# Optimization experiments

Hardware: AMD Instinct MI355X
Metric: run time of the kernel (lower is better)

## Reference

```python
import jax, jax.numpy as jnp
import numpy as np

B, T, NM = 128, 2048, 8  # batch, nSteps, nMaxwell


def setup_inputs() -> dict:
    key = jax.random.key(0)
    k1, k2, k3 = jax.random.split(key, 3)
    S_e = jax.random.normal(k1, (B, T, 3, 3), dtype=jnp.float32)
    # strictly increasing times per batch element
    dt = jax.random.uniform(k2, (B, T), minval=0.01, maxval=0.1, dtype=jnp.float32)
    t = jnp.cumsum(dt, axis=1)
    # [tau_1..tau_nM, g_infy, g_1..g_nM] -> last dim 2*NM + 1
    PronyParams = jax.random.uniform(k3, (B, T, 2 * NM + 1), minval=0.1, maxval=1.0, dtype=jnp.float32)
    return {"S_e": S_e, "t": t, "PronyParams": PronyParams}


def reference(S_e, t, PronyParams):
    """Viscoelastic 2nd Piola-Kirchhoff stress via recursive Prony update.

    S_e:         [B, T, 3, 3] instantaneous elastic stress
    t:           [B, T] time
    PronyParams: [B, T, 2*nM+1] (relaxation times tau then coefficients g)
    Returns (S, S_infy, Q_sum), each [B, T, 3, 3].
    """
    nM = PronyParams.shape[-1] // 2
    tau = PronyParams[..., :nM]                      # [B,T,nM]
    g = PronyParams[..., nM:]                        # [B,T,nM+1]
    g = g / jnp.sum(g, axis=-1, keepdims=True)
    g_infy = g[..., 0:1]                             # [B,T,1]
    g_i = g[..., 1:]                                 # [B,T,nM]

    Bsz = S_e.shape[0]
    # time-major scan inputs
    xs = (
        jnp.swapaxes(t, 0, 1),      # [T,B]
        jnp.swapaxes(S_e, 0, 1),    # [T,B,3,3]
        jnp.swapaxes(tau, 0, 1),    # [T,B,nM]
        jnp.swapaxes(g_i, 0, 1),    # [T,B,nM]
    )
    init = (
        jnp.zeros((Bsz, nM, 3, 3), S_e.dtype),  # Q_0
        -t[:, 1],                                # t_prev (as in original initializer)
        jnp.zeros((Bsz, 3, 3), S_e.dtype),       # S_prev
        tau[:, 0],
        g_i[:, 0],
    )

    def step(carry, x):
        Q_p, t_p, S_p, tau_p, g_p = carry
        t_c, S_c, tau_c, g_c = x
        g_bar = 0.5 * (g_c + g_p)                 # [B,nM]
        tau_bar = 0.5 * (tau_c + tau_p)           # [B,nM]
        dt = (t_c - t_p)[:, None]                 # [B,1]
        e = jnp.exp(-0.5 * dt / tau_bar)          # exp(-dt/(2 tau_bar))
        term1 = (e * e)[..., None, None]          # exp(-dt/tau_bar), [B,nM,1,1]
        term2 = (e * g_bar)[..., None, None]      # [B,nM,1,1]
        dS = (S_c - S_p)[:, None]                 # [B,1,3,3]
        Q = term1 * Q_p + term2 * dS              # [B,nM,3,3]
        return (Q, t_c, S_c, tau_c, g_c), Q

    _, Qs = jax.lax.scan(step, init, xs)          # [T,B,nM,3,3]
    Q_sum = jnp.swapaxes(jnp.sum(Qs, axis=2), 0, 1)  # [B,T,3,3]
    S_infy = g_infy[..., None] * S_e              # [B,T,1,1] * [B,T,3,3]
    S = S_infy + Q_sum
    return (S, S_infy, Q_sum)
```

## Files before the change

### kernel.cpp

```cpp
#include <hip/hip_runtime.h>

#define T_LEN 2048
#define NMODE 8
#define NPP   17

template <int L, int G>
__global__ __launch_bounds__(256, 8)
void fused(const float* __restrict__ Se,
           const float* __restrict__ tt,
           const float* __restrict__ pp,
           float* __restrict__ out,
           float* __restrict__ spine,
           unsigned* __restrict__ flags,
           unsigned* __restrict__ ticket,
           int B) {
    constexpr int NSTEP = G * L;
    constexpr int TILES = T_LEN / NSTEP;
    constexpr int RW    = NSTEP + 1;
    constexpr int NT    = 256;
    constexpr int RAW_SZ = RW * NPP;
    constexpr int SROW   = NSTEP + 4;
    constexpr int QT_SZ  = 9 * SROW;
    constexpr int CA_K   = L * 8 + 4;
    constexpr int UNION_SZ = (RAW_SZ > QT_SZ + G * CA_K) ? RAW_SZ
                                                         : (QT_SZ + G * CA_K);
    constexpr int AC_K  = L * 16 + 4;
    constexpr int O_AC  = UNION_SZ;
    constexpr int OV_ZREL = 0;
    constexpr int OV_PP   = G * 72;
    constexpr int OV_Z    = OV_PP + G * 8;
    constexpr int OV_R    = OV_Z + G * 72;
    constexpr int OV_P    = OV_R + G * 72;
    static_assert(OV_P + G * 8 <= G * AC_K, "overlay fits in AC region");
    constexpr int O_T   = O_AC + G * AC_K;
    constexpr int O_INV = O_T + RW;
    constexpr int O_GI  = O_INV + RW;
    constexpr int TOTAL = O_GI + RW;
    static_assert(TOTAL * 4 <= 20480, "LDS must allow 8 blocks/CU");
    static_assert(L == 16, "epilogue uses t>>4 / t&15");

    __shared__ __align__(16) float sm[TOTAL];
    float* s_raw  = sm;
    float* s_qT   = sm;
    float* s_ca   = sm + QT_SZ;
    float* s_AC   = sm + O_AC;
    float* s_Zrel = sm + O_AC + OV_ZREL;
    float* s_Pp   = sm + O_AC + OV_PP;
    float* s_Z    = sm + O_AC + OV_Z;
    float* s_R    = sm + O_AC + OV_R;
    float* s_P    = sm + O_AC + OV_P;
    float* s_t    = sm + O_T;
    float* s_inv  = sm + O_INV;
    float* s_gi   = sm + O_GI;

    const int tid = threadIdx.x;

    __shared__ unsigned s_vid;
    if (tid == 0) s_vid = atomicAdd(ticket, 1u);
    __syncthreads();
    const int vid  = (int)(s_vid % (unsigned)(B * TILES));
    const int tile = vid / B;
    const int b    = vid % B;

    const int base = tile * NSTEP;
    const int off  = (base == 0) ? 0 : 1;
    const int r0   = (base == 0) ? 0 : base - 1;

    {
        const float* pr = pp + ((size_t)b * T_LEN + r0) * NPP;
        for (int i = tid; i < RW * NPP; i += NT) s_raw[i] = pr[i];
        const float* tr = tt + (size_t)b * T_LEN + r0;
        for (int i = tid; i < RW; i += NT) s_t[i] = tr[i];
    }
    __syncthreads();

    for (int i = tid; i < RW; i += NT) {
        float gs = 0.f;
        #pragma unroll
        for (int k = 8; k < NPP; ++k) gs += s_raw[i * NPP + k];
        float iv = __builtin_amdgcn_rcpf(gs);
        s_inv[i] = iv;
        s_gi[i]  = s_raw[i * NPP + 8] * iv;
    }
    __syncthreads();

    for (int i = tid; i < NSTEP * 8; i += NT) {
        int m  = i & 7;
        int ts = i >> 3;
        int rc = ts + off;
        bool first = (base == 0) && (ts == 0);
        int rp = first ? rc : rc - 1;
        float tau_c = s_raw[rc * NPP + m];
        float tau_p = s_raw[rp * NPP + m];
        float gqh_c = 0.5f * s_raw[rc * NPP + 9 + m] * s_inv[rc];
        float gqh_p = 0.5f * s_raw[rp * NPP + 9 + m] * s_inv[rp];
        float t_c = s_t[rc];
        float t_p = first ? -s_t[1] : s_t[rp];
        float ee  = __expf((t_p - t_c) * __builtin_amdgcn_rcpf(tau_c + tau_p));
        int kk = ts / L, sl = ts % L;
        s_AC[kk * AC_K + sl * 16 + m]     = ee * ee;
        s_AC[kk * AC_K + sl * 16 + 8 + m] = ee * (gqh_c + gqh_p);
    }
    __syncthreads();

    float Q[8] = {0,0,0,0,0,0,0,0};
    float cumA_c = 1.f;
    if (tid < 72) {
        const int k = tid / 9;
        const int e = tid - k * 9;
        const float* Sg = Se + (size_t)b * T_LEN * 9 + e;
        const int gbase = base + k * L;

        float dS[L];
        {
            float prev = (base == 0 && k == 0) ? 0.f
                                               : Sg[(size_t)(gbase - 1) * 9];
            #pragma unroll
            for (int s = 0; s < L; ++s) {
                float cur = Sg[(size_t)(gbase + s) * 9];
                dS[s] = cur - prev;
                prev = cur;
            }
        }

        const float4* acp = (const float4*)(s_AC + k * AC_K);
        #pragma unroll
        for (int s = 0; s < L; ++s) {
            float4 a0 = acp[4*s], a1 = acp[4*s+1];
            float4 c0v = acp[4*s+2], c1v = acp[4*s+3];
            float d = dS[s];
            Q[0] = a0.x*Q[0] + c0v.x*d;  Q[1] = a0.y*Q[1] + c0v.y*d;
            Q[2] = a0.z*Q[2] + c0v.z*d;  Q[3] = a0.w*Q[3] + c0v.w*d;
            Q[4] = a1.x*Q[4] + c1v.x*d;  Q[5] = a1.y*Q[5] + c1v.y*d;
            Q[6] = a1.z*Q[6] + c1v.z*d;  Q[7] = a1.w*Q[7] + c1v.w*d;
            float qs = ((Q[0]+Q[1])+(Q[2]+Q[3])) + ((Q[4]+Q[5])+(Q[6]+Q[7]));
            s_qT[e * SROW + (k * L + s)] = qs;
        }
    } else if (tid >= 192) {
        const int u = tid - 192;
        const int k = u >> 3;
        const int m = u & 7;
        #pragma unroll
        for (int s = 0; s < L; ++s) {
            cumA_c *= s_AC[k * AC_K + s * 16 + m];
            s_ca[k * CA_K + s * 8 + m] = cumA_c;
        }
    }
    __syncthreads();

    if (tid < 72) {
        float4* r4 = (float4*)(s_R + 8 * tid);
        r4[0] = make_float4(Q[0], Q[1], Q[2], Q[3]);
        r4[1] = make_float4(Q[4], Q[5], Q[6], Q[7]);
    } else if (tid >= 192) {
        s_P[tid - 192] = cumA_c;
    }
    __syncthreads();

    if (tid < 72) {
        const int e = tid >> 3;
        const int m = tid & 7;
        float z = 0.f, pprod = 1.f;
        #pragma unroll
        for (int k = 0; k < G; ++k) {
            s_Zrel[k * 72 + tid] = z;
            if (e == 0) s_Pp[k * 8 + m] = pprod;
            float Pk = s_P[k * 8 + m];
            z = Pk * z + s_R[k * 72 + tid];
            pprod *= Pk;
        }
        if (tile != TILES - 1) {
            float* sp = spine + ((size_t)b * TILES + tile) * 80;
            __hip_atomic_store(sp + 8 + tid, z, __ATOMIC_RELAXED,
                               __HIP_MEMORY_SCOPE_AGENT);
            if (e == 0)
                __hip_atomic_store(sp + m, pprod, __ATOMIC_RELAXED,
                                   __HIP_MEMORY_SCOPE_AGENT);
        }
    }
    if (tile != TILES - 1)
        asm volatile("s_waitcnt vmcnt(0)" ::: "memory");
    __syncthreads();

    if (tile != TILES - 1 && tid == 0)
        __hip_atomic_store(&flags[(size_t)b * TILES + tile], 1u,
                           __ATOMIC_RELAXED, __HIP_MEMORY_SCOPE_AGENT);

    const size_t nOut = (size_t)B * T_LEN * 9;
    float* o0 = out + ((size_t)b * T_LEN + base) * 9;
    float* o1 = o0 + nOut;
    float* o2 = o0 + 2 * nOut;
    const float4* sv4 = (const float4*)(Se + ((size_t)b * T_LEN + base) * 9);
    for (int i4 = tid; i4 < NSTEP * 9 / 4; i4 += NT) {
        float4 sv = sv4[i4];
        int i = i4 * 4;
        float f0 = s_gi[(i    ) / 9 + off] * sv.x;
        float f1 = s_gi[(i + 1) / 9 + off] * sv.y;
        float f2 = s_gi[(i + 2) / 9 + off] * sv.z;
        float f3 = s_gi[(i + 3) / 9 + off] * sv.w;
        ((float4*)o1)[i4] = make_float4(f0, f1, f2, f3);
    }

    if (tile > 0 && tid < 64) {
        bool done = (tid >= tile);
        while (!__all(done)) {
            if (!done) {
                unsigned f = __hip_atomic_load(
                    &flags[(size_t)b * TILES + tid],
                    __ATOMIC_RELAXED, __HIP_MEMORY_SCOPE_AGENT);
                done = (f != 0u);
                if (!done) __builtin_amdgcn_s_sleep(1);
            }
        }
    }
    __syncthreads();

    float zin = 0.f;
    if (tid < 72 && tile > 0) {
        const int m = tid & 7;
        const float* spb = spine + (size_t)b * TILES * 80;
        float Pv[TILES - 1], Rv[TILES - 1];
        #pragma unroll
        for (int j = 0; j < TILES - 1; ++j) {
            if (j < tile) {
                Pv[j] = __hip_atomic_load(spb + j * 80 + m,
                                          __ATOMIC_RELAXED,
                                          __HIP_MEMORY_SCOPE_AGENT);
                Rv[j] = __hip_atomic_load(spb + j * 80 + 8 + tid,
                                          __ATOMIC_RELAXED,
                                          __HIP_MEMORY_SCOPE_AGENT);
            }
        }
        #pragma unroll
        for (int j = 0; j < TILES - 1; ++j)
            if (j < tile) zin = Pv[j] * zin + Rv[j];
    }

    if (tid < 72) {
        const int m = tid & 7;
        #pragma unroll
        for (int k = 0; k < G; ++k)
            s_Z[k * 72 + tid] = s_Pp[k * 8 + m] * zin + s_Zrel[k * 72 + tid];
    }
    __syncthreads();

    for (int i4 = tid; i4 < NSTEP * 9 / 4; i4 += NT) {
        float4 sv = sv4[i4];
        const float svc[4] = {sv.x, sv.y, sv.z, sv.w};
        int i = i4 * 4;
        float q[4], f[4];
        #pragma unroll
        for (int j = 0; j < 4; ++j) {
            int idx = i + j;
            int t = idx / 9, e = idx - t * 9;
            int rc = t + off;
            int k = t >> 4, s = t & 15;
            const float* caT = &s_ca[k * CA_K + s * 8];
            const float* zE  = &s_Z[k * 72 + e * 8];
            float cr = 0.f;
            #pragma unroll
            for (int m = 0; m < NMODE; ++m) cr += caT[m] * zE[m];
            q[j] = s_qT[e * SROW + t] + cr;
            f[j] = s_gi[rc] * svc[j];
        }
        ((float4*)o2)[i4] = make_float4(q[0], q[1], q[2], q[3]);
        ((float4*)o0)[i4] = make_float4(f[0]+q[0], f[1]+q[1],
                                        f[2]+q[2], f[3]+q[3]);
    }
}

extern "C" void kernel_launch(void* const* d_in, const int* in_sizes, int n_in,
                              void* d_out, int out_size, void* d_ws, size_t ws_size,
                              hipStream_t stream) {
    const float* Se = (const float*)d_in[0];
    const float* tt = (const float*)d_in[1];
    const float* pp = (const float*)d_in[2];
    float* out = (float*)d_out;

    int B = in_sizes[1] / T_LEN;

    constexpr int L = 16;
    constexpr int G = 8;
    constexpr int NSTEP = G * L;
    constexpr int TILES = T_LEN / NSTEP;

    unsigned* ticket = (unsigned*)d_ws;
    unsigned* flags  = ticket + 1;
    size_t ctl_bytes = (size_t)(1 + B * TILES) * sizeof(unsigned);
    size_t spine_off = (ctl_bytes + 15) & ~(size_t)15;
    float* spine = (float*)((char*)d_ws + spine_off);

    hipMemsetAsync(d_ws, 0, ctl_bytes, stream);

    fused<L, G><<<B * TILES, dim3(256), 0, stream>>>(
        Se, tt, pp, out, spine, flags, ticket, B);
}
```

Measured before the change: 118.9 us.

## Overlap S_infy output with scan, stripe ticket atomics, drop LDS param staging

```diff
diff --git a/kernel.cpp b/kernel.cpp
--- a/kernel.cpp
+++ b/kernel.cpp
@@ -18,29 +18,24 @@
     constexpr int TILES = T_LEN / NSTEP;
     constexpr int RW    = NSTEP + 1;
     constexpr int NT    = 256;
-    constexpr int RAW_SZ = RW * NPP;
-    constexpr int SROW   = NSTEP + 4;
-    constexpr int QT_SZ  = 9 * SROW;
-    constexpr int CA_K   = L * 8 + 4;
-    constexpr int UNION_SZ = (RAW_SZ > QT_SZ + G * CA_K) ? RAW_SZ
-                                                         : (QT_SZ + G * CA_K);
+    constexpr int SROW  = NSTEP + 4;
+    constexpr int QT_SZ = 9 * SROW;
+    constexpr int CA_K  = L * 8 + 4;
     constexpr int AC_K  = L * 16 + 4;
-    constexpr int O_AC  = UNION_SZ;
+    constexpr int O_AC  = QT_SZ + G * CA_K;
     constexpr int OV_ZREL = 0;
     constexpr int OV_PP   = G * 72;
     constexpr int OV_Z    = OV_PP + G * 8;
     constexpr int OV_R    = OV_Z + G * 72;
     constexpr int OV_P    = OV_R + G * 72;
     static_assert(OV_P + G * 8 <= G * AC_K, "overlay fits in AC region");
-    constexpr int O_T   = O_AC + G * AC_K;
-    constexpr int O_INV = O_T + RW;
+    constexpr int O_INV = O_AC + G * AC_K;
     constexpr int O_GI  = O_INV + RW;
     constexpr int TOTAL = O_GI + RW;
     static_assert(TOTAL * 4 <= 20480, "LDS must allow 8 blocks/CU");
     static_assert(L == 16, "epilogue uses t>>4 / t&15");
 
     __shared__ __align__(16) float sm[TOTAL];
-    float* s_raw  = sm;
     float* s_qT   = sm;
     float* s_ca   = sm + QT_SZ;
     float* s_AC   = sm + O_AC;
@@ -49,14 +44,17 @@
     float* s_Z    = sm + O_AC + OV_Z;
     float* s_R    = sm + O_AC + OV_R;
     float* s_P    = sm + O_AC + OV_P;
-    float* s_t    = sm + O_T;
     float* s_inv  = sm + O_INV;
     float* s_gi   = sm + O_GI;
 
     const int tid = threadIdx.x;
 
     __shared__ unsigned s_vid;
-    if (tid == 0) s_vid = atomicAdd(ticket, 1u);
+    if (tid == 0) {
+        unsigned stripe = (unsigned)blockIdx.x & 7u;
+        unsigned idx = atomicAdd(&ticket[stripe], 1u);
+        s_vid = idx * 8u + stripe;
+    }
     __syncthreads();
     const int vid  = (int)(s_vid % (unsigned)(B * TILES));
     const int tile = vid / B;
@@ -66,21 +64,17 @@
     const int off  = (base == 0) ? 0 : 1;
     const int r0   = (base == 0) ? 0 : base - 1;
 
-    {
-        const float* pr = pp + ((size_t)b * T_LEN + r0) * NPP;
-        for (int i = tid; i < RW * NPP; i += NT) s_raw[i] = pr[i];
-        const float* tr = tt + (size_t)b * T_LEN + r0;
-        for (int i = tid; i < RW; i += NT) s_t[i] = tr[i];
-    }
-    __syncthreads();
+    const float* ppb = pp + ((size_t)b * T_LEN + r0) * NPP;
+    const float* ttb = tt + (size_t)b * T_LEN + r0;
 
     for (int i = tid; i < RW; i += NT) {
+        const float* gp = ppb + i * NPP + 8;
         float gs = 0.f;
         #pragma unroll
-        for (int k = 8; k < NPP; ++k) gs += s_raw[i * NPP + k];
+        for (int k = 0; k < 9; ++k) gs += gp[k];
         float iv = __builtin_amdgcn_rcpf(gs);
         s_inv[i] = iv;
-        s_gi[i]  = s_raw[i * NPP + 8] * iv;
+        s_gi[i]  = gp[0] * iv;
     }
     __syncthreads();
 
@@ -90,18 +84,24 @@
         int rc = ts + off;
         bool first = (base == 0) && (ts == 0);
         int rp = first ? rc : rc - 1;
-        float tau_c = s_raw[rc * NPP + m];
-        float tau_p = s_raw[rp * NPP + m];
-        float gqh_c = 0.5f * s_raw[rc * NPP + 9 + m] * s_inv[rc];
-        float gqh_p = 0.5f * s_raw[rp * NPP + 9 + m] * s_inv[rp];
-        float t_c = s_t[rc];
-        float t_p = first ? -s_t[1] : s_t[rp];
+        float tau_c = ppb[rc * NPP + m];
+        float tau_p = ppb[rp * NPP + m];
+        float gqh_c = 0.5f * ppb[rc * NPP + 9 + m] * s_inv[rc];
+        float gqh_p = 0.5f * ppb[rp * NPP + 9 + m] * s_inv[rp];
+        float t_c = ttb[rc];
+        float t_p = first ? -ttb[1] : ttb[rp];
         float ee  = __expf((t_p - t_c) * __builtin_amdgcn_rcpf(tau_c + tau_p));
         int kk = ts / L, sl = ts % L;
         s_AC[kk * AC_K + sl * 16 + m]     = ee * ee;
         s_AC[kk * AC_K + sl * 16 + 8 + m] = ee * (gqh_c + gqh_p);
     }
     __syncthreads();
+
+    const size_t nOut = (size_t)B * T_LEN * 9;
+    float* o0 = out + ((size_t)b * T_LEN + base) * 9;
+    float* o1 = o0 + nOut;
+    float* o2 = o0 + 2 * nOut;
+    const float4* sv4 = (const float4*)(Se + ((size_t)b * T_LEN + base) * 9);
 
     float Q[8] = {0,0,0,0,0,0,0,0};
     float cumA_c = 1.f;
@@ -136,7 +136,17 @@
             float qs = ((Q[0]+Q[1])+(Q[2]+Q[3])) + ((Q[4]+Q[5])+(Q[6]+Q[7]));
             s_qT[e * SROW + (k * L + s)] = qs;
         }
-    } else if (tid >= 192) {
+    } else if (tid < 192) {
+        for (int i4 = tid - 72; i4 < NSTEP * 9 / 4; i4 += 120) {
+            float4 sv = sv4[i4];
+            int i = i4 * 4;
+            float f0 = s_gi[(i    ) / 9 + off] * sv.x;
+            float f1 = s_gi[(i + 1) / 9 + off] * sv.y;
+            float f2 = s_gi[(i + 2) / 9 + off] * sv.z;
+            float f3 = s_gi[(i + 3) / 9 + off] * sv.w;
+            ((float4*)o1)[i4] = make_float4(f0, f1, f2, f3);
+        }
+    } else {
         const int u = tid - 192;
         const int k = u >> 3;
         const int m = u & 7;
@@ -185,21 +195,6 @@
     if (tile != TILES - 1 && tid == 0)
         __hip_atomic_store(&flags[(size_t)b * TILES + tile], 1u,
                            __ATOMIC_RELAXED, __HIP_MEMORY_SCOPE_AGENT);
-
-    const size_t nOut = (size_t)B * T_LEN * 9;
-    float* o0 = out + ((size_t)b * T_LEN + base) * 9;
-    float* o1 = o0 + nOut;
-    float* o2 = o0 + 2 * nOut;
-    const float4* sv4 = (const float4*)(Se + ((size_t)b * T_LEN + base) * 9);
-    for (int i4 = tid; i4 < NSTEP * 9 / 4; i4 += NT) {
-        float4 sv = sv4[i4];
-        int i = i4 * 4;
-        float f0 = s_gi[(i    ) / 9 + off] * sv.x;
-        float f1 = s_gi[(i + 1) / 9 + off] * sv.y;
-        float f2 = s_gi[(i + 2) / 9 + off] * sv.z;
-        float f3 = s_gi[(i + 3) / 9 + off] * sv.w;
-        ((float4*)o1)[i4] = make_float4(f0, f1, f2, f3);
-    }
 
     if (tile > 0 && tid < 64) {
         bool done = (tid >= tile);
@@ -255,11 +250,12 @@
             int t = idx / 9, e = idx - t * 9;
             int rc = t + off;
             int k = t >> 4, s = t & 15;
-            const float* caT = &s_ca[k * CA_K + s * 8];
-            const float* zE  = &s_Z[k * 72 + e * 8];
-            float cr = 0.f;
-            #pragma unroll
-            for (int m = 0; m < NMODE; ++m) cr += caT[m] * zE[m];
+            const float4* ca4 = (const float4*)(s_ca + k * CA_K + s * 8);
+            const float4* z4  = (const float4*)(s_Z + k * 72 + e * 8);
+            float4 cA = ca4[0], cB = ca4[1];
+            float4 zA = z4[0],  zB = z4[1];
+            float cr = ((cA.x*zA.x + cA.y*zA.y) + (cA.z*zA.z + cA.w*zA.w))
+                     + ((cB.x*zB.x + cB.y*zB.y) + (cB.z*zB.z + cB.w*zB.w));
             q[j] = s_qT[e * SROW + t] + cr;
             f[j] = s_gi[rc] * svc[j];
         }
@@ -285,8 +281,8 @@
     constexpr int TILES = T_LEN / NSTEP;
 
     unsigned* ticket = (unsigned*)d_ws;
-    unsigned* flags  = ticket + 1;
-    size_t ctl_bytes = (size_t)(1 + B * TILES) * sizeof(unsigned);
+    unsigned* flags  = ticket + 8;
+    size_t ctl_bytes = (size_t)(8 + B * TILES) * sizeof(unsigned);
     size_t spine_off = (ctl_bytes + 15) & ~(size_t)15;
     float* spine = (float*)((char*)d_ws + spine_off);
 
```

Result: no change. 118.8 us (-0.1%).
